# Kernel optimization log

Hardware: AMD Instinct MI355X
Metric: run time of the kernel (lower is better)

The kernel has to match this reference:

```python
import jax, jax.numpy as jnp
import numpy as np

N_NODES = 1_000_000
N_EDGES = 16_000_000
N_FEAT = 128
NUM_GRAPHS = 8192


def setup_inputs() -> dict:
    key = jax.random.key(0)
    k_x, k_e, k_b, k_w, k_pw, k_pb = jax.random.split(key, 6)
    x = jax.random.normal(k_x, (N_NODES, N_FEAT), dtype=jnp.float32)
    edge_index = jax.random.randint(k_e, (2, N_EDGES), 0, N_NODES, dtype=jnp.int64)
    batch = jnp.sort(jax.random.randint(k_b, (N_NODES,), 0, NUM_GRAPHS, dtype=jnp.int64))
    # GCNConv lin weight (F -> 1, no bias), xavier-ish scale
    W = jax.random.normal(k_w, (N_FEAT, 1), dtype=jnp.float32) * (6.0 / (N_FEAT + 1)) ** 0.5
    # post_pool Linear(1, 1, bias=True)
    pp_w = jax.random.normal(k_pw, (1, 1), dtype=jnp.float32)
    pp_b = jax.random.normal(k_pb, (1,), dtype=jnp.float32) * 0.1
    return {"x": x, "W": W, "pp_w": pp_w, "pp_b": pp_b,
            "edge_index": edge_index, "batch": batch}


def reference(x, W, pp_w, pp_b, edge_index, batch):
    N = x.shape[0]
    h = x @ W  # [N, 1] — tiny feature after GCNConv projection
    # add self-loops (PyG GCNConv default)
    loops = jnp.arange(N, dtype=edge_index.dtype)
    src = jnp.concatenate([edge_index[0], loops])  # message sources (col j)
    dst = jnp.concatenate([edge_index[1], loops])  # aggregation targets (row i)
    # symmetric degree normalization: deg over targets incl. self-loops
    deg = jax.ops.segment_sum(jnp.ones(src.shape[0], dtype=h.dtype), dst,
                              num_segments=N)
    dinv = jnp.where(deg > 0, jax.lax.rsqrt(deg), 0.0)
    norm = dinv[src] * dinv[dst]  # [E+N]
    # gather -> normalize -> scatter-add
    agg = jax.ops.segment_sum(norm[:, None] * h[src], dst, num_segments=N)  # [N,1]
    # global_add_pool by graph id
    pooled = jax.ops.segment_sum(agg, batch, num_segments=NUM_GRAPHS)  # [G,1]
    return pooled @ pp_w.T + pp_b  # Linear(1,1)
```

## Files before the change

### kernel.cpp

```cpp
#include <hip/hip_runtime.h>
#include <hip/hip_fp16.h>

#define NUM_GRAPHS 8192
#define BSHIFT 12
#define BSIZE 4096
#define CHUNK 4096
#define NGRP 32

__global__ void node_h_kernel(const float* __restrict__ x,
                              const float* __restrict__ W,
                              float* __restrict__ h, int N) {
    int gwave = (blockIdx.x * blockDim.x + threadIdx.x) >> 6;
    int lane = threadIdx.x & 63;
    int half = lane >> 5;
    int l32  = lane & 31;
    int total_waves = (gridDim.x * blockDim.x) >> 6;
    float4 wv = ((const float4*)W)[l32];
    for (int node = gwave * 2 + half; node < N; node += total_waves * 2) {
        float4 xv = ((const float4*)(x + (size_t)node * 128))[l32];
        float v = xv.x * wv.x + xv.y * wv.y + xv.z * wv.z + xv.w * wv.w;
        #pragma unroll
        for (int d = 16; d >= 1; d >>= 1) v += __shfl_xor(v, d);
        if (l32 == 0) h[node] = v;
    }
}

__global__ void __launch_bounds__(256)
pair_scatter_kernel(const int* __restrict__ src, const int* __restrict__ dst,
                    int E, int nchunks, int NBUK, int capG,
                    unsigned* __restrict__ cursor, unsigned* __restrict__ slab) {
    __shared__ unsigned cnt[256];
    __shared__ unsigned lbase[256];
    __shared__ unsigned sbase[256];
    __shared__ unsigned staged[CHUNK];
    __shared__ unsigned char sbuck[CHUNK];
    __shared__ unsigned s_tot;

    const int4* s4 = (const int4*)src;
    const int4* d4 = (const int4*)dst;
    int E4 = E >> 2;
    int tid = threadIdx.x;
    int g = blockIdx.x & (NGRP - 1);

    for (int chunk = blockIdx.x; chunk < nchunks; chunk += gridDim.x) {
        cnt[tid] = 0; __syncthreads();
        int b4 = chunk * (CHUNK / 4);
        int4 vd[4], vs[4];
        unsigned short r[16];
        #pragma unroll
        for (int k = 0; k < 4; ++k) {
            int idx = b4 + k * 256 + tid;
            if (idx < E4) { vd[k] = d4[idx]; vs[k] = s4[idx]; }
            else          { vd[k] = make_int4(-1, -1, -1, -1); }
        }
        #pragma unroll
        for (int k = 0; k < 4; ++k) {
            if (vd[k].x >= 0) {
                r[4*k+0] = (unsigned short)atomicAdd(&cnt[vd[k].x >> BSHIFT], 1u);
                r[4*k+1] = (unsigned short)atomicAdd(&cnt[vd[k].y >> BSHIFT], 1u);
                r[4*k+2] = (unsigned short)atomicAdd(&cnt[vd[k].z >> BSHIFT], 1u);
                r[4*k+3] = (unsigned short)atomicAdd(&cnt[vd[k].w >> BSHIFT], 1u);
            }
        }
        __syncthreads();
        lbase[tid] = cnt[tid]; __syncthreads();
        #pragma unroll
        for (int off = 1; off < 256; off <<= 1) {
            unsigned a = (tid >= off) ? lbase[tid - off] : 0u;
            __syncthreads();
            lbase[tid] += a;
            __syncthreads();
        }
        if (tid == 255) s_tot = lbase[255];
        if (tid < NBUK && cnt[tid]) sbase[tid] = atomicAdd(&cursor[g * 256 + tid], cnt[tid]);
        unsigned excl = lbase[tid] - cnt[tid];
        __syncthreads();
        lbase[tid] = excl;
        __syncthreads();

        #pragma unroll
        for (int k = 0; k < 4; ++k) {
            if (vd[k].x >= 0) {
                int d0 = vd[k].x, d1 = vd[k].y, d2 = vd[k].z, d3 = vd[k].w;
                unsigned b0 = (unsigned)d0 >> BSHIFT, b1 = (unsigned)d1 >> BSHIFT;
                unsigned b2 = (unsigned)d2 >> BSHIFT, b3 = (unsigned)d3 >> BSHIFT;
                unsigned p0 = lbase[b0] + r[4*k+0];
                unsigned p1 = lbase[b1] + r[4*k+1];
                unsigned p2 = lbase[b2] + r[4*k+2];
                unsigned p3 = lbase[b3] + r[4*k+3];
                staged[p0] = ((unsigned)(d0 & (BSIZE - 1)) << 20) | (unsigned)vs[k].x;
                staged[p1] = ((unsigned)(d1 & (BSIZE - 1)) << 20) | (unsigned)vs[k].y;
                staged[p2] = ((unsigned)(d2 & (BSIZE - 1)) << 20) | (unsigned)vs[k].z;
                staged[p3] = ((unsigned)(d3 & (BSIZE - 1)) << 20) | (unsigned)vs[k].w;
                sbuck[p0] = (unsigned char)b0;
                sbuck[p1] = (unsigned char)b1;
                sbuck[p2] = (unsigned char)b2;
                sbuck[p3] = (unsigned char)b3;
            }
        }
        __syncthreads();

        unsigned tot = s_tot;
        for (unsigned pos = tid; pos < tot; pos += 256) {
            unsigned b = sbuck[pos];
            unsigned gp = sbase[b] + (pos - lbase[b]);
            if (gp < (unsigned)capG)
                slab[((size_t)g * NBUK + b) * capG + gp] = staged[pos];
        }
        __syncthreads();
    }
    if (blockIdx.x == 0 && tid < (E & 3)) {
        int i = (E & ~3) + tid;
        int d = dst[i];
        unsigned b = (unsigned)d >> BSHIFT;
        unsigned p = atomicAdd(&cursor[b], 1u);
        if (p < (unsigned)capG)
            slab[(size_t)b * capG + p] =
                ((unsigned)(d & (BSIZE - 1)) << 20) | (unsigned)src[i];
    }
}

__global__ void __launch_bounds__(1024)
hist_finalize_kernel(const unsigned* __restrict__ slab, int capG,
                     const unsigned* __restrict__ cursor,
                     const float* __restrict__ h, const int* __restrict__ batch,
                     unsigned short* __restrict__ hsh, unsigned* __restrict__ pkw,
                     int N, int NBUK) {
    __shared__ unsigned hist[BSIZE];
    int b = blockIdx.x, tid = threadIdx.x;
    for (int t = tid; t < BSIZE; t += 1024) hist[t] = 0;
    __syncthreads();
    for (int g = 0; g < NGRP; ++g) {
        unsigned n = cursor[g * 256 + b]; if (n > (unsigned)capG) n = capG;
        const unsigned* s = slab + ((size_t)g * NBUK + b) * capG;
        for (unsigned i = tid; i < n; i += 1024) atomicAdd(&hist[s[i] >> 20], 1u);
    }
    __syncthreads();
    int base = b << BSHIFT;
    int lim = N - base; if (lim > BSIZE) lim = BSIZE;
    for (int t = tid; t < lim; t += 1024) {
        float di = rsqrtf((float)(hist[t] + 1u));
        hsh[base + t] = __half_as_ushort(__float2half(di * h[base + t]));
        pkw[base + t] = ((unsigned)batch[base + t] << 16) |
                        __half_as_ushort(__float2half(di));
    }
}

__global__ void __launch_bounds__(1024)
aggregate_kernel(const unsigned* __restrict__ slab, int capG,
                 const unsigned* __restrict__ cursor,
                 const unsigned* __restrict__ pkw,
                 const unsigned short* __restrict__ hsh,
                 float* __restrict__ pooled, int N, int NBUK) {
    __shared__ float pool[NUM_GRAPHS];
    __shared__ unsigned pkw_s[BSIZE];
    int b = blockIdx.x, tid = threadIdx.x;
    int base = b << BSHIFT;
    int lim = N - base; if (lim > BSIZE) lim = BSIZE;

    for (int t = tid; t < NUM_GRAPHS; t += 1024) pool[t] = 0.0f;
    for (int t = tid; t < BSIZE; t += 1024) pkw_s[t] = (t < lim) ? pkw[base + t] : 0u;
    __syncthreads();

    for (int t = tid; t < lim; t += 1024) {
        unsigned w = pkw_s[t];
        float di = __half2float(__ushort_as_half((unsigned short)(w & 0xFFFFu)));
        float c = di * __half2float(__ushort_as_half(hsh[base + t]));
        atomicAdd(&pool[w >> 16], c);
    }

    for (int g = 0; g < NGRP; ++g) {
        unsigned n = cursor[g * 256 + b]; if (n > (unsigned)capG) n = capG;
        const unsigned* s = slab + ((size_t)g * NBUK + b) * capG;
        for (unsigned i = tid; i < n; i += 1024) {
            unsigned e = s[i];
            unsigned w = pkw_s[e >> 20];
            float hv = __half2float(__ushort_as_half(hsh[e & 0xFFFFFu]));
            float di = __half2float(__ushort_as_half((unsigned short)(w & 0xFFFFu)));
            atomicAdd(&pool[w >> 16], hv * di);
        }
    }
    __syncthreads();

    int g_lo = (int)(pkw_s[0] >> 16);
    int g_hi = (lim > 0) ? (int)(pkw_s[lim - 1] >> 16) : g_lo;
    for (int g = g_lo + tid; g <= g_hi; g += 1024) atomicAdd(&pooled[g], pool[g]);
}

__global__ void out_kernel(const float* __restrict__ pooled,
                           const float* __restrict__ pp_w,
                           const float* __restrict__ pp_b,
                           float* __restrict__ out) {
    int g = blockIdx.x * blockDim.x + threadIdx.x;
    if (g < NUM_GRAPHS) out[g] = pooled[g] * pp_w[0] + pp_b[0];
}

__global__ void deg_atomic_kernel(const int* __restrict__ dst, int E,
                                  unsigned* __restrict__ deg) {
    int tid = blockIdx.x * blockDim.x + threadIdx.x;
    int stride = gridDim.x * blockDim.x;
    for (int i = tid; i < E; i += stride) atomicAdd(&deg[dst[i]], 1u);
}

__global__ void node_fb_kernel(const float* __restrict__ x,
                               const float* __restrict__ W,
                               const unsigned* __restrict__ deg,
                               const int* __restrict__ batch,
                               unsigned short* __restrict__ hsh,
                               unsigned* __restrict__ pkw, int N) {
    int gtid = blockIdx.x * blockDim.x + threadIdx.x;
    int wave = gtid >> 6;
    int lane = threadIdx.x & 63;
    int half = lane >> 5;
    int l32  = lane & 31;
    int node = wave * 2 + half;
    if (node >= N) return;
    float4 xv = ((const float4*)(x + (size_t)node * 128))[l32];
    float4 wv = ((const float4*)W)[l32];
    float v = xv.x * wv.x + xv.y * wv.y + xv.z * wv.z + xv.w * wv.w;
// ... 23 lines not shown
                   float* __restrict__ pooled) {
    __shared__ float pool[NUM_GRAPHS];
    for (int g = threadIdx.x; g < NUM_GRAPHS; g += 512) pool[g] = 0.0f;
    __syncthreads();
    int tid = blockIdx.x * 512 + threadIdx.x;
    int stride = gridDim.x * 512;
    for (int i = tid; i < E; i += stride) {
        unsigned w = pkw[dst[i]];
        float c = __half2float(__ushort_as_half(hsh[src[i]])) *
                  __half2float(__ushort_as_half((unsigned short)(w & 0xFFFFu)));
        atomicAdd(&pool[w >> 16], c);
    }
    __syncthreads();
    for (int g = threadIdx.x; g < NUM_GRAPHS; g += 512)
        if (pool[g] != 0.0f) atomicAdd(&pooled[g], pool[g]);
}

extern "C" void kernel_launch(void* const* d_in, const int* in_sizes, int n_in,
                              void* d_out, int out_size, void* d_ws, size_t ws_size,
                              hipStream_t stream) {
    const float* x    = (const float*)d_in[0];
    const float* W    = (const float*)d_in[1];
    const float* pp_w = (const float*)d_in[2];
    const float* pp_b = (const float*)d_in[3];
    const int*   ei   = (const int*)d_in[4];
    const int*   batch= (const int*)d_in[5];
    float* out = (float*)d_out;

    const int E = in_sizes[4] / 2;
    const int N = in_sizes[5];
    const int* src = ei;
    const int* dst = ei + E;
    int NBUK = (N + BSIZE - 1) >> BSHIFT;

    char* ws = (char*)d_ws;
    size_t off = 0;
    auto alloc = [&](size_t bytes) {
        size_t o = off; off = (off + bytes + 255) & ~(size_t)255; return o;
    };
    size_t h_off      = alloc((size_t)N * 4);
    size_t hsh_off    = alloc((size_t)N * 2);
    size_t pkw_off    = alloc((size_t)N * 4);
    size_t pooled_off = alloc((size_t)NUM_GRAPHS * 4);
    size_t cursor_off = alloc((size_t)NGRP * 256 * 4);

    int meanG = E / (NBUK * NGRP) + 1;
    int capG = meanG + meanG / 8 + 512;
    size_t slab_off = alloc((size_t)NGRP * NBUK * (size_t)capG * 4);

    bool slab_ok = (NBUK <= 256) && (N <= (1 << 20)) && (off <= ws_size);

    float*          h      = (float*)(ws + h_off);
    unsigned*       deg    = (unsigned*)(ws + h_off);
    unsigned short* hsh    = (unsigned short*)(ws + hsh_off);
    unsigned*       pkw    = (unsigned*)(ws + pkw_off);
    float*          pooled = (float*)(ws + pooled_off);
    unsigned*       cursor = (unsigned*)(ws + cursor_off);
    unsigned*       slab   = (unsigned*)(ws + slab_off);

    hipMemsetAsync(pooled, 0, (size_t)NUM_GRAPHS * 4, stream);

    if (slab_ok) {
        hipMemsetAsync(cursor, 0, (size_t)NGRP * 256 * 4, stream);
        int E4 = E >> 2;
        int nchunks = (E4 + (CHUNK / 4 - 1)) / (CHUNK / 4);
        int grid = nchunks < 4096 ? nchunks : 4096;
        pair_scatter_kernel<<<grid, 256, 0, stream>>>(src, dst, E, nchunks, NBUK,
                                                      capG, cursor, slab);
        node_h_kernel<<<8192, 256, 0, stream>>>(x, W, h, N);
        hist_finalize_kernel<<<NBUK, 1024, 0, stream>>>(slab, capG, cursor, h,
                                                        batch, hsh, pkw, N, NBUK);
        aggregate_kernel<<<NBUK, 1024, 0, stream>>>(slab, capG, cursor, pkw, hsh,
                                                    pooled, N, NBUK);
    } else {
        hipMemsetAsync(deg, 0, (size_t)N * 4, stream);
        deg_atomic_kernel<<<2048, 256, 0, stream>>>(dst, E, deg);
        int node_blocks = (N + 7) / 8;
        node_fb_kernel<<<node_blocks, 256, 0, stream>>>(x, W, deg, batch, hsh, pkw, N);
        pool_self_fb_kernel<<<(N + 255) / 256, 256, 0, stream>>>(hsh, pkw, pooled, N);
        edge_direct_kernel<<<512, 512, 0, stream>>>(src, dst, E, hsh, pkw, pooled);
    }

    out_kernel<<<(NUM_GRAPHS + 255) / 256, 256, 0, stream>>>(pooled, pp_w, pp_b, out);
}
```

Before: 305.3 us.

## Fuse edge bucketing and node projection into one persistent work-stealing kernel

Merges the edge bucket-scatter kernel and the x@W node projection kernel into a single persistent kernel of 1536 blocks. Each block pulls work from two atomic counters, doing KREP edge chunks and then one node tile in turn, so the latency-bound scatter overlaps with the bandwidth-bound read of x. The two memsets are merged into one over a contiguous zeroed region that also holds the new work counters. The exchange is an extra global atomic per work item and a fixed grid size, and it may change how slab writes are grouped across blocks, since g still comes from blockIdx.

```diff
diff --git a/kernel.cpp b/kernel.cpp
--- a/kernel.cpp
+++ b/kernel.cpp
@@ -6,108 +6,126 @@
 #define BSIZE 4096
 #define CHUNK 4096
 #define NGRP 32
-
-__global__ void node_h_kernel(const float* __restrict__ x,
-                              const float* __restrict__ W,
-                              float* __restrict__ h, int N) {
-    int gwave = (blockIdx.x * blockDim.x + threadIdx.x) >> 6;
-    int lane = threadIdx.x & 63;
-    int half = lane >> 5;
-    int l32  = lane & 31;
-    int total_waves = (gridDim.x * blockDim.x) >> 6;
-    float4 wv = ((const float4*)W)[l32];
-    for (int node = gwave * 2 + half; node < N; node += total_waves * 2) {
-        float4 xv = ((const float4*)(x + (size_t)node * 128))[l32];
-        float v = xv.x * wv.x + xv.y * wv.y + xv.z * wv.z + xv.w * wv.w;
-        #pragma unroll
-        for (int d = 16; d >= 1; d >>= 1) v += __shfl_xor(v, d);
-        if (l32 == 0) h[node] = v;
-    }
-}
+#define HTILE 2048
+#define KREP 8
 
 __global__ void __launch_bounds__(256)
-pair_scatter_kernel(const int* __restrict__ src, const int* __restrict__ dst,
-                    int E, int nchunks, int NBUK, int capG,
-                    unsigned* __restrict__ cursor, unsigned* __restrict__ slab) {
+fused_scatter_h_kernel(const int* __restrict__ src, const int* __restrict__ dst,
+                       int E, int nchunks, int NBUK, int capG,
+                       unsigned* __restrict__ cursor, unsigned* __restrict__ slab,
+                       const float* __restrict__ x, const float* __restrict__ W,
+                       float* __restrict__ h, int N, int ntiles,
+                       unsigned* __restrict__ ccur, unsigned* __restrict__ hcur) {
     __shared__ unsigned cnt[256];
     __shared__ unsigned lbase[256];
     __shared__ unsigned sbase[256];
     __shared__ unsigned staged[CHUNK];
     __shared__ unsigned char sbuck[CHUNK];
     __shared__ unsigned s_tot;
+    __shared__ unsigned s_work;
 
     const int4* s4 = (const int4*)src;
     const int4* d4 = (const int4*)dst;
-    int E4 = E >> 2;
-    int tid = threadIdx.x;
-    int g = blockIdx.x & (NGRP - 1);
-
-    for (int chunk = blockIdx.x; chunk < nchunks; chunk += gridDim.x) {
-        cnt[tid] = 0; __syncthreads();
-        int b4 = chunk * (CHUNK / 4);
-        int4 vd[4], vs[4];
-        unsigned short r[16];
-        #pragma unroll
-        for (int k = 0; k < 4; ++k) {
-            int idx = b4 + k * 256 + tid;
-            if (idx < E4) { vd[k] = d4[idx]; vs[k] = s4[idx]; }
-            else          { vd[k] = make_int4(-1, -1, -1, -1); }
+    const int E4 = E >> 2;
+    const int tid = threadIdx.x;
+    const int g = blockIdx.x & (NGRP - 1);
+
+    const int wv = tid >> 6, hhalf = (tid >> 5) & 1, l32 = tid & 31;
+    const float4 wvec = ((const float4*)W)[l32];
+
+    bool cdone = false, hdone = false;
+    while (!(cdone && hdone)) {
+        for (int rep = 0; rep < KREP && !cdone; ++rep) {
+            if (tid == 0) s_work = atomicAdd(ccur, 1u);
+            __syncthreads();
+            unsigned chunk = s_work;
+            __syncthreads();
+            if (chunk >= (unsigned)nchunks) { cdone = true; continue; }
+
+            cnt[tid] = 0; __syncthreads();
+            int b4 = (int)chunk * (CHUNK / 4);
+            int4 vd[4], vs[4];
+            unsigned short r[16];
+            #pragma unroll
+            for (int k = 0; k < 4; ++k) {
+                int idx = b4 + k * 256 + tid;
+                if (idx < E4) { vd[k] = d4[idx]; vs[k] = s4[idx]; }
+                else          { vd[k] = make_int4(-1, -1, -1, -1); }
+            }
+            #pragma unroll
+            for (int k = 0; k < 4; ++k) {
+                if (vd[k].x >= 0) {
+                    r[4*k+0] = (unsigned short)atomicAdd(&cnt[vd[k].x >> BSHIFT], 1u);
+                    r[4*k+1] = (unsigned short)atomicAdd(&cnt[vd[k].y >> BSHIFT], 1u);
+                    r[4*k+2] = (unsigned short)atomicAdd(&cnt[vd[k].z >> BSHIFT], 1u);
+                    r[4*k+3] = (unsigned short)atomicAdd(&cnt[vd[k].w >> BSHIFT], 1u);
+                }
+            }
+            __syncthreads();
+            lbase[tid] = cnt[tid]; __syncthreads();
+            #pragma unroll
+            for (int off = 1; off < 256; off <<= 1) {
+                unsigned a = (tid >= off) ? lbase[tid - off] : 0u;
+                __syncthreads();
+                lbase[tid] += a;
+                __syncthreads();
+            }
+            if (tid == 255) s_tot = lbase[255];
+            if (tid < NBUK && cnt[tid])
+                sbase[tid] = atomicAdd(&cursor[g * 256 + tid], cnt[tid]);
+            unsigned excl = lbase[tid] - cnt[tid];
+            __syncthreads();
+            lbase[tid] = excl;
+            __syncthreads();
+
+            #pragma unroll
+            for (int k = 0; k < 4; ++k) {
+                if (vd[k].x >= 0) {
+                    int d0 = vd[k].x, d1 = vd[k].y, d2 = vd[k].z, d3 = vd[k].w;
+                    unsigned b0 = (unsigned)d0 >> BSHIFT, b1 = (unsigned)d1 >> BSHIFT;
+                    unsigned b2 = (unsigned)d2 >> BSHIFT, b3 = (unsigned)d3 >> BSHIFT;
+                    unsigned p0 = lbase[b0] + r[4*k+0];
+                    unsigned p1 = lbase[b1] + r[4*k+1];
+                    unsigned p2 = lbase[b2] + r[4*k+2];
+                    unsigned p3 = lbase[b3] + r[4*k+3];
+                    staged[p0] = ((unsigned)(d0 & (BSIZE-1)) << 20) | (unsigned)vs[k].x;
+                    staged[p1] = ((unsigned)(d1 & (BSIZE-1)) << 20) | (unsigned)vs[k].y;
+                    staged[p2] = ((unsigned)(d2 & (BSIZE-1)) << 20) | (unsigned)vs[k].z;
+                    staged[p3] = ((unsigned)(d3 & (BSIZE-1)) << 20) | (unsigned)vs[k].w;
+                    sbuck[p0] = (unsigned char)b0;
+                    sbuck[p1] = (unsigned char)b1;
+                    sbuck[p2] = (unsigned char)b2;
+                    sbuck[p3] = (unsigned char)b3;
+                }
+            }
+            __syncthreads();
+            unsigned tot = s_tot;
+            for (unsigned pos = tid; pos < tot; pos += 256) {
+                unsigned b = sbuck[pos];
+                unsigned gp = sbase[b] + (pos - lbase[b]);
+                if (gp < (unsigned)capG)
+                    slab[((size_t)g * NBUK + b) * capG + gp] = staged[pos];
+            }
+            __syncthreads();
         }
-        #pragma unroll
-        for (int k = 0; k < 4; ++k) {
-            if (vd[k].x >= 0) {
-                r[4*k+0] = (unsigned short)atomicAdd(&cnt[vd[k].x >> BSHIFT], 1u);
-                r[4*k+1] = (unsigned short)atomicAdd(&cnt[vd[k].y >> BSHIFT], 1u);
-                r[4*k+2] = (unsigned short)atomicAdd(&cnt[vd[k].z >> BSHIFT], 1u);
-                r[4*k+3] = (unsigned short)atomicAdd(&cnt[vd[k].w >> BSHIFT], 1u);
+        if (!hdone) {
+            if (tid == 0) s_work = atomicAdd(hcur, 1u);
+            __syncthreads();
+            unsigned t = s_work;
+            __syncthreads();
+            if (t >= (unsigned)ntiles) { hdone = true; continue; }
+            int tbase = (int)t * HTILE;
+            for (int nn = wv * 2 + hhalf; nn < HTILE; nn += 8) {
+                int node = tbase + nn;
+                if (node < N) {
+                    float4 xv = ((const float4*)(x + (size_t)node * 128))[l32];
+                    float v = xv.x*wvec.x + xv.y*wvec.y + xv.z*wvec.z + xv.w*wvec.w;
+                    #pragma unroll
+                    for (int d = 16; d >= 1; d >>= 1) v += __shfl_xor(v, d);
+                    if (l32 == 0) h[node] = v;
+                }
             }
         }
-        __syncthreads();
-        lbase[tid] = cnt[tid]; __syncthreads();
-        #pragma unroll
-        for (int off = 1; off < 256; off <<= 1) {
-            unsigned a = (tid >= off) ? lbase[tid - off] : 0u;
-            __syncthreads();
-            lbase[tid] += a;
-            __syncthreads();
-        }
-        if (tid == 255) s_tot = lbase[255];
-        if (tid < NBUK && cnt[tid]) sbase[tid] = atomicAdd(&cursor[g * 256 + tid], cnt[tid]);
-        unsigned excl = lbase[tid] - cnt[tid];
-        __syncthreads();
-        lbase[tid] = excl;
-        __syncthreads();
-
-        #pragma unroll
-        for (int k = 0; k < 4; ++k) {
-            if (vd[k].x >= 0) {
-                int d0 = vd[k].x, d1 = vd[k].y, d2 = vd[k].z, d3 = vd[k].w;
-                unsigned b0 = (unsigned)d0 >> BSHIFT, b1 = (unsigned)d1 >> BSHIFT;
-                unsigned b2 = (unsigned)d2 >> BSHIFT, b3 = (unsigned)d3 >> BSHIFT;
-                unsigned p0 = lbase[b0] + r[4*k+0];
-                unsigned p1 = lbase[b1] + r[4*k+1];
-                unsigned p2 = lbase[b2] + r[4*k+2];
-                unsigned p3 = lbase[b3] + r[4*k+3];
-                staged[p0] = ((unsigned)(d0 & (BSIZE - 1)) << 20) | (unsigned)vs[k].x;
-                staged[p1] = ((unsigned)(d1 & (BSIZE - 1)) << 20) | (unsigned)vs[k].y;
-                staged[p2] = ((unsigned)(d2 & (BSIZE - 1)) << 20) | (unsigned)vs[k].z;
-                staged[p3] = ((unsigned)(d3 & (BSIZE - 1)) << 20) | (unsigned)vs[k].w;
-                sbuck[p0] = (unsigned char)b0;
-                sbuck[p1] = (unsigned char)b1;
-                sbuck[p2] = (unsigned char)b2;
-                sbuck[p3] = (unsigned char)b3;
-            }
-        }
-        __syncthreads();
-
-        unsigned tot = s_tot;
-        for (unsigned pos = tid; pos < tot; pos += 256) {
-            unsigned b = sbuck[pos];
-            unsigned gp = sbase[b] + (pos - lbase[b]);
-            if (gp < (unsigned)capG)
-                slab[((size_t)g * NBUK + b) * capG + gp] = staged[pos];
-        }
-        __syncthreads();
     }
     if (blockIdx.x == 0 && tid < (E & 3)) {
         int i = (E & ~3) + tid;
@@ -116,7 +134,7 @@
         unsigned p = atomicAdd(&cursor[b], 1u);
         if (p < (unsigned)capG)
             slab[(size_t)b * capG + p] =
-                ((unsigned)(d & (BSIZE - 1)) << 20) | (unsigned)src[i];
+                ((unsigned)(d & (BSIZE-1)) << 20) | (unsigned)src[i];
     }
 }
 
@@ -168,7 +186,6 @@
         float c = di * __half2float(__ushort_as_half(hsh[base + t]));
         atomicAdd(&pool[w >> 16], c);
     }
-
     for (int g = 0; g < NGRP; ++g) {
         unsigned n = cursor[g * 256 + b]; if (n > (unsigned)capG) n = capG;
         const unsigned* s = slab + ((size_t)g * NBUK + b) * capG;
@@ -181,7 +198,6 @@
         }
     }
     __syncthreads();
-
     int g_lo = (int)(pkw_s[0] >> 16);
     int g_hi = (lim > 0) ? (int)(pkw_s[lim - 1] >> 16) : g_lo;
     for (int g = g_lo + tid; g <= g_hi; g += 1024) atomicAdd(&pooled[g], pool[g]);
@@ -280,11 +296,17 @@
     auto alloc = [&](size_t bytes) {
         size_t o = off; off = (off + bytes + 255) & ~(size_t)255; return o;
     };
-    size_t h_off      = alloc((size_t)N * 4);
-    size_t hsh_off    = alloc((size_t)N * 2);
-    size_t pkw_off    = alloc((size_t)N * 4);
-    size_t pooled_off = alloc((size_t)NUM_GRAPHS * 4);
-    size_t cursor_off = alloc((size_t)NGRP * 256 * 4);
+    size_t zero_bytes = (size_t)NUM_GRAPHS * 4 + (size_t)NGRP * 256 * 4 + 256;
+    size_t zero_off   = alloc(zero_bytes);
+    float*    pooled = (float*)(ws + zero_off);
+    unsigned* cursor = (unsigned*)(ws + zero_off + (size_t)NUM_GRAPHS * 4);
+    unsigned* ccur   = (unsigned*)(ws + zero_off + (size_t)NUM_GRAPHS * 4
+                                   + (size_t)NGRP * 256 * 4);
+    unsigned* hcur   = ccur + 1;
+
+    size_t h_off    = alloc((size_t)N * 4);
+    size_t hsh_off  = alloc((size_t)N * 2);
+    size_t pkw_off  = alloc((size_t)N * 4);
 
     int meanG = E / (NBUK * NGRP) + 1;
     int capG = meanG + meanG / 8 + 512;
@@ -292,24 +314,21 @@
 
     bool slab_ok = (NBUK <= 256) && (N <= (1 << 20)) && (off <= ws_size);
 
-    float*          h      = (float*)(ws + h_off);
-    unsigned*       deg    = (unsigned*)(ws + h_off);
-    unsigned short* hsh    = (unsigned short*)(ws + hsh_off);
-    unsigned*       pkw    = (unsigned*)(ws + pkw_off);
-    float*          pooled = (float*)(ws + pooled_off);
-    unsigned*       cursor = (unsigned*)(ws + cursor_off);
-    unsigned*       slab   = (unsigned*)(ws + slab_off);
-
-    hipMemsetAsync(pooled, 0, (size_t)NUM_GRAPHS * 4, stream);
+    float*          h    = (float*)(ws + h_off);
+    unsigned*       deg  = (unsigned*)(ws + h_off);
+    unsigned short* hsh  = (unsigned short*)(ws + hsh_off);
+    unsigned*       pkw  = (unsigned*)(ws + pkw_off);
+    unsigned*       slab = (unsigned*)(ws + slab_off);
+
+    hipMemsetAsync(ws + zero_off, 0, zero_bytes, stream);
 
     if (slab_ok) {
-        hipMemsetAsync(cursor, 0, (size_t)NGRP * 256 * 4, stream);
         int E4 = E >> 2;
         int nchunks = (E4 + (CHUNK / 4 - 1)) / (CHUNK / 4);
-        int grid = nchunks < 4096 ? nchunks : 4096;
-        pair_scatter_kernel<<<grid, 256, 0, stream>>>(src, dst, E, nchunks, NBUK,
-                                                      capG, cursor, slab);
-        node_h_kernel<<<8192, 256, 0, stream>>>(x, W, h, N);
+        int ntiles  = (N + HTILE - 1) / HTILE;
+        fused_scatter_h_kernel<<<1536, 256, 0, stream>>>(
+            src, dst, E, nchunks, NBUK, capG, cursor, slab,
+            x, W, h, N, ntiles, ccur, hcur);
         hist_finalize_kernel<<<NBUK, 1024, 0, stream>>>(slab, capG, cursor, h,
                                                         batch, hsh, pkw, N, NBUK);
         aggregate_kernel<<<NBUK, 1024, 0, stream>>>(slab, capG, cursor, pkw, hsh,
```

After: 437.5 us. 1.43x slower.

## Replace atomic-cursor bucket slabs with deterministic count-scan-scatter partitioning

Applied to the files above, without the earlier changes.

Replaces the single-pass scatter into 32 over-provisioned per-group slabs with a three-stage counting sort. Per-chunk bucket counts are gathered first, then scanned per bucket and globally, and the scatter writes each edge to an exact offset in a compact E-sized slab. The hist and aggregate kernels then read one contiguous range per bucket instead of looping over 32 groups. This drops global cursor atomics, capacity clipping and the slab padding, at the cost of reading dst twice and adding extra small kernel launches. The local prefix scan also moves from a block-wide shared-memory scan to a single-wave shuffle scan.

```diff
diff --git a/kernel.cpp b/kernel.cpp
--- a/kernel.cpp
+++ b/kernel.cpp
@@ -5,7 +5,175 @@
 #define BSHIFT 12
 #define BSIZE 4096
 #define CHUNK 4096
-#define NGRP 32
+#define NTHR 256
+
+__global__ void __launch_bounds__(NTHR)
+count_kernel(const int* __restrict__ dst, int E, int nchunks,
+             unsigned* __restrict__ countsT) {
+    __shared__ unsigned cnt[256];
+    int tid = threadIdx.x;
+    int E4 = E >> 2;
+    const int4* d4 = (const int4*)dst;
+    for (int chunk = blockIdx.x; chunk < nchunks; chunk += gridDim.x) {
+        cnt[tid] = 0; __syncthreads();
+        int b4 = chunk * (CHUNK / 4);
+        #pragma unroll
+        for (int k = 0; k < 4; ++k) {
+            int idx = b4 + k * NTHR + tid;
+            if (idx < E4) {
+                int4 v = d4[idx];
+                atomicAdd(&cnt[v.x >> BSHIFT], 1u);
+                atomicAdd(&cnt[v.y >> BSHIFT], 1u);
+                atomicAdd(&cnt[v.z >> BSHIFT], 1u);
+                atomicAdd(&cnt[v.w >> BSHIFT], 1u);
+            }
+        }
+        if (chunk == nchunks - 1 && tid < (E & 3))
+            atomicAdd(&cnt[dst[E4 * 4 + tid] >> BSHIFT], 1u);
+        __syncthreads();
+        countsT[(size_t)chunk * 256 + tid] = cnt[tid];
+        __syncthreads();
+    }
+}
+
+__global__ void __launch_bounds__(64)
+chunkscan_kernel(const unsigned* __restrict__ countsT, int nchunks,
+                 unsigned* __restrict__ base2T, unsigned* __restrict__ total) {
+    int b = blockIdx.x, lane = threadIdx.x;
+    unsigned run = 0;
+    for (int c0 = 0; c0 < nchunks; c0 += 64) {
+        int c = c0 + lane;
+        unsigned v = (c < nchunks) ? countsT[(size_t)c * 256 + b] : 0u;
+        unsigned s = v;
+        #pragma unroll
+        for (int off = 1; off < 64; off <<= 1) {
+            unsigned o = __shfl_up(s, off);
+            if (lane >= off) s += o;
+        }
+        if (c < nchunks) base2T[(size_t)c * 256 + b] = run + s - v;
+        run += __shfl(s, 63);
+    }
+    if (lane == 0) total[b] = run;
+}
+
+__global__ void gbase_kernel(const unsigned* __restrict__ total,
+                             unsigned* __restrict__ gbase) {
+    __shared__ unsigned s[256];
+    int tid = threadIdx.x;
+    unsigned v = total[tid];
+    s[tid] = v; __syncthreads();
+    #pragma unroll
+    for (int off = 1; off < 256; off <<= 1) {
+        unsigned a = (tid >= off) ? s[tid - off] : 0u;
+        __syncthreads();
+        s[tid] += a;
+        __syncthreads();
+    }
+    gbase[tid] = s[tid] - v;
+    if (tid == 255) gbase[256] = s[255];
+}
+
+__global__ void __launch_bounds__(NTHR)
+scatter_kernel(const int* __restrict__ src, const int* __restrict__ dst,
+               int E, int nchunks,
+               const unsigned* __restrict__ base2T,
+               const unsigned* __restrict__ gbase,
+               unsigned* __restrict__ slab) {
+    __shared__ unsigned cnt[256];
+    __shared__ unsigned lbase[256];
+    __shared__ unsigned sbase[256];
+    __shared__ unsigned staged[CHUNK + 4];
+    __shared__ unsigned char sbuck[CHUNK + 4];
+    __shared__ unsigned s_tot;
+
+    const int4* s4 = (const int4*)src;
+    const int4* d4 = (const int4*)dst;
+    const int E4 = E >> 2;
+    const int tid = threadIdx.x;
+
+    for (int chunk = blockIdx.x; chunk < nchunks; chunk += gridDim.x) {
+        cnt[tid] = 0; __syncthreads();
+        int b4 = chunk * (CHUNK / 4);
+        int4 vd[4], vs[4];
+        unsigned short r[16];
+        #pragma unroll
+        for (int k = 0; k < 4; ++k) {
+            int idx = b4 + k * NTHR + tid;
+            if (idx < E4) { vd[k] = d4[idx]; vs[k] = s4[idx]; }
+            else          { vd[k] = make_int4(-1, -1, -1, -1); }
+        }
+        #pragma unroll
+        for (int k = 0; k < 4; ++k) {
+            if (vd[k].x >= 0) {
+                r[4*k+0] = (unsigned short)atomicAdd(&cnt[vd[k].x >> BSHIFT], 1u);
+                r[4*k+1] = (unsigned short)atomicAdd(&cnt[vd[k].y >> BSHIFT], 1u);
+                r[4*k+2] = (unsigned short)atomicAdd(&cnt[vd[k].z >> BSHIFT], 1u);
+                r[4*k+3] = (unsigned short)atomicAdd(&cnt[vd[k].w >> BSHIFT], 1u);
+            }
+        }
+        int tr = -1, tsrc = 0, tdlo = 0, tb = 0;
+        if (chunk == nchunks - 1 && tid < (E & 3)) {
+            int i = E4 * 4 + tid;
+            int d = dst[i];
+            tb = d >> BSHIFT;
+            tr = (int)atomicAdd(&cnt[tb], 1u);
+            tdlo = d & (BSIZE - 1);
+            tsrc = src[i];
+        }
+        __syncthreads();
+        sbase[tid] = gbase[tid] + base2T[(size_t)chunk * 256 + tid];
+        if (tid < 64) {
+            unsigned run = 0;
+            for (int c0 = 0; c0 < 256; c0 += 64) {
+                unsigned v = cnt[c0 + tid];
+                unsigned s = v;
+                #pragma unroll
+                for (int off = 1; off < 64; off <<= 1) {
+                    unsigned o = __shfl_up(s, off);
+                    if (tid >= off) s += o;
+                }
+                lbase[c0 + tid] = run + s - v;
+                run += __shfl(s, 63);
+            }
+            if (tid == 0) s_tot = run;
+        }
+        __syncthreads();
+
+        #pragma unroll
+        for (int k = 0; k < 4; ++k) {
+            if (vd[k].x >= 0) {
+                int d0 = vd[k].x, d1 = vd[k].y, d2 = vd[k].z, d3 = vd[k].w;
+                unsigned b0 = (unsigned)d0 >> BSHIFT, b1 = (unsigned)d1 >> BSHIFT;
+                unsigned b2 = (unsigned)d2 >> BSHIFT, b3 = (unsigned)d3 >> BSHIFT;
+                unsigned p0 = lbase[b0] + r[4*k+0];
+                unsigned p1 = lbase[b1] + r[4*k+1];
+                unsigned p2 = lbase[b2] + r[4*k+2];
+                unsigned p3 = lbase[b3] + r[4*k+3];
+                staged[p0] = ((unsigned)(d0 & (BSIZE-1)) << 20) | (unsigned)vs[k].x;
+                staged[p1] = ((unsigned)(d1 & (BSIZE-1)) << 20) | (unsigned)vs[k].y;
+                staged[p2] = ((unsigned)(d2 & (BSIZE-1)) << 20) | (unsigned)vs[k].z;
+                staged[p3] = ((unsigned)(d3 & (BSIZE-1)) << 20) | (unsigned)vs[k].w;
+                sbuck[p0] = (unsigned char)b0;
+                sbuck[p1] = (unsigned char)b1;
+                sbuck[p2] = (unsigned char)b2;
+                sbuck[p3] = (unsigned char)b3;
+            }
+        }
+        if (tr >= 0) {
+            unsigned p = lbase[tb] + (unsigned)tr;
+            staged[p] = ((unsigned)tdlo << 20) | (unsigned)tsrc;
+            sbuck[p] = (unsigned char)tb;
+        }
+        __syncthreads();
+
+        unsigned tot = s_tot;
+        for (unsigned pos = tid; pos < tot; pos += NTHR) {
+            unsigned b = sbuck[pos];
+            slab[sbase[b] + (pos - lbase[b])] = staged[pos];
+        }
+        __syncthreads();
+    }
+}
 
 __global__ void node_h_kernel(const float* __restrict__ x,
                               const float* __restrict__ W,
@@ -25,116 +193,19 @@
     }
 }
 
-__global__ void __launch_bounds__(256)
-pair_scatter_kernel(const int* __restrict__ src, const int* __restrict__ dst,
-                    int E, int nchunks, int NBUK, int capG,
-                    unsigned* __restrict__ cursor, unsigned* __restrict__ slab) {
-    __shared__ unsigned cnt[256];
-    __shared__ unsigned lbase[256];
-    __shared__ unsigned sbase[256];
-    __shared__ unsigned staged[CHUNK];
-    __shared__ unsigned char sbuck[CHUNK];
-    __shared__ unsigned s_tot;
-
-    const int4* s4 = (const int4*)src;
-    const int4* d4 = (const int4*)dst;
-    int E4 = E >> 2;
-    int tid = threadIdx.x;
-    int g = blockIdx.x & (NGRP - 1);
-
-    for (int chunk = blockIdx.x; chunk < nchunks; chunk += gridDim.x) {
-        cnt[tid] = 0; __syncthreads();
-        int b4 = chunk * (CHUNK / 4);
-        int4 vd[4], vs[4];
-        unsigned short r[16];
-        #pragma unroll
-        for (int k = 0; k < 4; ++k) {
-            int idx = b4 + k * 256 + tid;
-            if (idx < E4) { vd[k] = d4[idx]; vs[k] = s4[idx]; }
-            else          { vd[k] = make_int4(-1, -1, -1, -1); }
-        }
-        #pragma unroll
-        for (int k = 0; k < 4; ++k) {
-            if (vd[k].x >= 0) {
-                r[4*k+0] = (unsigned short)atomicAdd(&cnt[vd[k].x >> BSHIFT], 1u);
-                r[4*k+1] = (unsigned short)atomicAdd(&cnt[vd[k].y >> BSHIFT], 1u);
-                r[4*k+2] = (unsigned short)atomicAdd(&cnt[vd[k].z >> BSHIFT], 1u);
-                r[4*k+3] = (unsigned short)atomicAdd(&cnt[vd[k].w >> BSHIFT], 1u);
-            }
-        }
-        __syncthreads();
-        lbase[tid] = cnt[tid]; __syncthreads();
-        #pragma unroll
-        for (int off = 1; off < 256; off <<= 1) {
-            unsigned a = (tid >= off) ? lbase[tid - off] : 0u;
-            __syncthreads();
-            lbase[tid] += a;
-            __syncthreads();
-        }
-        if (tid == 255) s_tot = lbase[255];
-        if (tid < NBUK && cnt[tid]) sbase[tid] = atomicAdd(&cursor[g * 256 + tid], cnt[tid]);
-        unsigned excl = lbase[tid] - cnt[tid];
-        __syncthreads();
-        lbase[tid] = excl;
-        __syncthreads();
-
-        #pragma unroll
-        for (int k = 0; k < 4; ++k) {
-            if (vd[k].x >= 0) {
-                int d0 = vd[k].x, d1 = vd[k].y, d2 = vd[k].z, d3 = vd[k].w;
-                unsigned b0 = (unsigned)d0 >> BSHIFT, b1 = (unsigned)d1 >> BSHIFT;
-                unsigned b2 = (unsigned)d2 >> BSHIFT, b3 = (unsigned)d3 >> BSHIFT;
-                unsigned p0 = lbase[b0] + r[4*k+0];
-                unsigned p1 = lbase[b1] + r[4*k+1];
-                unsigned p2 = lbase[b2] + r[4*k+2];
-                unsigned p3 = lbase[b3] + r[4*k+3];
-                staged[p0] = ((unsigned)(d0 & (BSIZE - 1)) << 20) | (unsigned)vs[k].x;
-                staged[p1] = ((unsigned)(d1 & (BSIZE - 1)) << 20) | (unsigned)vs[k].y;
-                staged[p2] = ((unsigned)(d2 & (BSIZE - 1)) << 20) | (unsigned)vs[k].z;
-                staged[p3] = ((unsigned)(d3 & (BSIZE - 1)) << 20) | (unsigned)vs[k].w;
-                sbuck[p0] = (unsigned char)b0;
-                sbuck[p1] = (unsigned char)b1;
-                sbuck[p2] = (unsigned char)b2;
-                sbuck[p3] = (unsigned char)b3;
-            }
-        }
-        __syncthreads();
-
-        unsigned tot = s_tot;
-        for (unsigned pos = tid; pos < tot; pos += 256) {
-            unsigned b = sbuck[pos];
-            unsigned gp = sbase[b] + (pos - lbase[b]);
-            if (gp < (unsigned)capG)
-                slab[((size_t)g * NBUK + b) * capG + gp] = staged[pos];
-        }
-        __syncthreads();
-    }
-    if (blockIdx.x == 0 && tid < (E & 3)) {
-        int i = (E & ~3) + tid;
-        int d = dst[i];
-        unsigned b = (unsigned)d >> BSHIFT;
-        unsigned p = atomicAdd(&cursor[b], 1u);
-        if (p < (unsigned)capG)
-            slab[(size_t)b * capG + p] =
-                ((unsigned)(d & (BSIZE - 1)) << 20) | (unsigned)src[i];
-    }
-}
-
 __global__ void __launch_bounds__(1024)
-hist_finalize_kernel(const unsigned* __restrict__ slab, int capG,
-                     const unsigned* __restrict__ cursor,
+hist_finalize_kernel(const unsigned* __restrict__ slab,
+                     const unsigned* __restrict__ gbase,
                      const float* __restrict__ h, const int* __restrict__ batch,
                      unsigned short* __restrict__ hsh, unsigned* __restrict__ pkw,
-                     int N, int NBUK) {
+                     int N) {
     __shared__ unsigned hist[BSIZE];
     int b = blockIdx.x, tid = threadIdx.x;
     for (int t = tid; t < BSIZE; t += 1024) hist[t] = 0;
     __syncthreads();
-    for (int g = 0; g < NGRP; ++g) {
-        unsigned n = cursor[g * 256 + b]; if (n > (unsigned)capG) n = capG;
-        const unsigned* s = slab + ((size_t)g * NBUK + b) * capG;
-        for (unsigned i = tid; i < n; i += 1024) atomicAdd(&hist[s[i] >> 20], 1u);
-    }
+    unsigned s0 = gbase[b], s1 = gbase[b + 1];
+    for (unsigned i = s0 + tid; i < s1; i += 1024)
+        atomicAdd(&hist[slab[i] >> 20], 1u);
     __syncthreads();
     int base = b << BSHIFT;
     int lim = N - base; if (lim > BSIZE) lim = BSIZE;
@@ -147,11 +218,11 @@
 }
 
 __global__ void __launch_bounds__(1024)
-aggregate_kernel(const unsigned* __restrict__ slab, int capG,
-                 const unsigned* __restrict__ cursor,
+aggregate_kernel(const unsigned* __restrict__ slab,
+                 const unsigned* __restrict__ gbase,
                  const unsigned* __restrict__ pkw,
                  const unsigned short* __restrict__ hsh,
-                 float* __restrict__ pooled, int N, int NBUK) {
+                 float* __restrict__ pooled, int N) {
     __shared__ float pool[NUM_GRAPHS];
     __shared__ unsigned pkw_s[BSIZE];
     int b = blockIdx.x, tid = threadIdx.x;
@@ -168,20 +239,15 @@
         float c = di * __half2float(__ushort_as_half(hsh[base + t]));
         atomicAdd(&pool[w >> 16], c);
     }
-
-    for (int g = 0; g < NGRP; ++g) {
-        unsigned n = cursor[g * 256 + b]; if (n > (unsigned)capG) n = capG;
-        const unsigned* s = slab + ((size_t)g * NBUK + b) * capG;
-        for (unsigned i = tid; i < n; i += 1024) {
-            unsigned e = s[i];
-            unsigned w = pkw_s[e >> 20];
-            float hv = __half2float(__ushort_as_half(hsh[e & 0xFFFFFu]));
-            float di = __half2float(__ushort_as_half((unsigned short)(w & 0xFFFFu)));
-            atomicAdd(&pool[w >> 16], hv * di);
-        }
-    }
-    __syncthreads();
-
+    unsigned s0 = gbase[b], s1 = gbase[b + 1];
+    for (unsigned i = s0 + tid; i < s1; i += 1024) {
+        unsigned e = slab[i];
+        unsigned w = pkw_s[e >> 20];
+        float hv = __half2float(__ushort_as_half(hsh[e & 0xFFFFFu]));
+        float di = __half2float(__ushort_as_half((unsigned short)(w & 0xFFFFu)));
+        atomicAdd(&pool[w >> 16], hv * di);
+    }
+    __syncthreads();
     int g_lo = (int)(pkw_s[0] >> 16);
     int g_hi = (lim > 0) ? (int)(pkw_s[lim - 1] >> 16) : g_lo;
     for (int g = g_lo + tid; g <= g_hi; g += 1024) atomicAdd(&pooled[g], pool[g]);
@@ -274,46 +340,50 @@
     const int* src = ei;
     const int* dst = ei + E;
     int NBUK = (N + BSIZE - 1) >> BSHIFT;
+    int nchunks = (E + CHUNK - 1) / CHUNK;
 
     char* ws = (char*)d_ws;
     size_t off = 0;
     auto alloc = [&](size_t bytes) {
         size_t o = off; off = (off + bytes + 255) & ~(size_t)255; return o;
     };
+    size_t pooled_off = alloc((size_t)NUM_GRAPHS * 4);
     size_t h_off      = alloc((size_t)N * 4);
     size_t hsh_off    = alloc((size_t)N * 2);
     size_t pkw_off    = alloc((size_t)N * 4);
-    size_t pooled_off = alloc((size_t)NUM_GRAPHS * 4);
-    size_t cursor_off = alloc((size_t)NGRP * 256 * 4);
-
-    int meanG = E / (NBUK * NGRP) + 1;
-    int capG = meanG + meanG / 8 + 512;
-    size_t slab_off = alloc((size_t)NGRP * NBUK * (size_t)capG * 4);
-
-    bool slab_ok = (NBUK <= 256) && (N <= (1 << 20)) && (off <= ws_size);
-
+    size_t counts_off = alloc((size_t)nchunks * 256 * 4);
+    size_t base2_off  = alloc((size_t)nchunks * 256 * 4);
+    size_t total_off  = alloc(256 * 4);
+    size_t gbase_off  = alloc(257 * 4);
+    size_t slab_off   = alloc((size_t)E * 4);
+
+    bool fast_ok = (NBUK <= 256) && (N <= (1 << 20)) && (off <= ws_size);
+
+    float*          pooled = (float*)(ws + pooled_off);
     float*          h      = (float*)(ws + h_off);
     unsigned*       deg    = (unsigned*)(ws + h_off);
     unsigned short* hsh    = (unsigned short*)(ws + hsh_off);
     unsigned*       pkw    = (unsigned*)(ws + pkw_off);
-    float*          pooled = (float*)(ws + pooled_off);
-    unsigned*       cursor = (unsigned*)(ws + cursor_off);
+    unsigned*       countsT= (unsigned*)(ws + counts_off);
+    unsigned*       base2T = (unsigned*)(ws + base2_off);
+    unsigned*       total  = (unsigned*)(ws + total_off);
+    unsigned*       gbase  = (unsigned*)(ws + gbase_off);
     unsigned*       slab   = (unsigned*)(ws + slab_off);
 
     hipMemsetAsync(pooled, 0, (size_t)NUM_GRAPHS * 4, stream);
 
-    if (slab_ok) {
-        hipMemsetAsync(cursor, 0, (size_t)NGRP * 256 * 4, stream);
-        int E4 = E >> 2;
-        int nchunks = (E4 + (CHUNK / 4 - 1)) / (CHUNK / 4);
-        int grid = nchunks < 4096 ? nchunks : 4096;
-        pair_scatter_kernel<<<grid, 256, 0, stream>>>(src, dst, E, nchunks, NBUK,
-                                                      capG, cursor, slab);
+    if (fast_ok) {
+        int grid_c = nchunks < 2048 ? nchunks : 2048;
+        count_kernel<<<grid_c, NTHR, 0, stream>>>(dst, E, nchunks, countsT);
+        chunkscan_kernel<<<256, 64, 0, stream>>>(countsT, nchunks, base2T, total);
+        gbase_kernel<<<1, 256, 0, stream>>>(total, gbase);
+        scatter_kernel<<<grid_c, NTHR, 0, stream>>>(src, dst, E, nchunks,
+                                                    base2T, gbase, slab);
         node_h_kernel<<<8192, 256, 0, stream>>>(x, W, h, N);
-        hist_finalize_kernel<<<NBUK, 1024, 0, stream>>>(slab, capG, cursor, h,
-                                                        batch, hsh, pkw, N, NBUK);
-        aggregate_kernel<<<NBUK, 1024, 0, stream>>>(slab, capG, cursor, pkw, hsh,
-                                                    pooled, N, NBUK);
+        hist_finalize_kernel<<<NBUK, 1024, 0, stream>>>(slab, gbase, h, batch,
+                                                        hsh, pkw, N);
+        aggregate_kernel<<<NBUK, 1024, 0, stream>>>(slab, gbase, pkw, hsh,
+                                                    pooled, N);
     } else {
         hipMemsetAsync(deg, 0, (size_t)N * 4, stream);
         deg_atomic_kernel<<<2048, 256, 0, stream>>>(dst, E, deg);
```

Result: slower. 351.8 us (+15.2%).

## Split histogram and aggregation across more blocks, fuse projection with normalization

Applied to the files above, without the earlier changes.

The degree histogram now runs in two blocks per bucket, each covering half the slab groups and writing partial degrees to two arrays. The node projection is fused with the rsqrt normalization and packing, so the separate h buffer and its round trip are gone. Aggregation runs four blocks per bucket with 8-way batched slab loads and gathers, and accumulates into a small replicated, padded shared-memory window of graph ids in place of a full 8192-entry pool. The aim is more parallelism over the ~245 buckets and less shared-atomic contention, at the cost of extra global atomics and a non-windowed fallback path.

```diff
diff --git a/kernel.cpp b/kernel.cpp
--- a/kernel.cpp
+++ b/kernel.cpp
@@ -6,24 +6,9 @@
 #define BSIZE 4096
 #define CHUNK 4096
 #define NGRP 32
-
-__global__ void node_h_kernel(const float* __restrict__ x,
-                              const float* __restrict__ W,
-                              float* __restrict__ h, int N) {
-    int gwave = (blockIdx.x * blockDim.x + threadIdx.x) >> 6;
-    int lane = threadIdx.x & 63;
-    int half = lane >> 5;
-    int l32  = lane & 31;
-    int total_waves = (gridDim.x * blockDim.x) >> 6;
-    float4 wv = ((const float4*)W)[l32];
-    for (int node = gwave * 2 + half; node < N; node += total_waves * 2) {
-        float4 xv = ((const float4*)(x + (size_t)node * 128))[l32];
-        float v = xv.x * wv.x + xv.y * wv.y + xv.z * wv.z + xv.w * wv.w;
-        #pragma unroll
-        for (int d = 16; d >= 1; d >>= 1) v += __shfl_xor(v, d);
-        if (l32 == 0) h[node] = v;
-    }
-}
+#define REPL 8
+#define WINDOW 256
+#define WPAD 257
 
 __global__ void __launch_bounds__(256)
 pair_scatter_kernel(const int* __restrict__ src, const int* __restrict__ dst,
@@ -72,7 +57,8 @@
             __syncthreads();
         }
         if (tid == 255) s_tot = lbase[255];
-        if (tid < NBUK && cnt[tid]) sbase[tid] = atomicAdd(&cursor[g * 256 + tid], cnt[tid]);
+        if (tid < NBUK && cnt[tid])
+            sbase[tid] = atomicAdd(&cursor[g * 256 + tid], cnt[tid]);
         unsigned excl = lbase[tid] - cnt[tid];
         __syncthreads();
         lbase[tid] = excl;
@@ -88,10 +74,10 @@
                 unsigned p1 = lbase[b1] + r[4*k+1];
                 unsigned p2 = lbase[b2] + r[4*k+2];
                 unsigned p3 = lbase[b3] + r[4*k+3];
-                staged[p0] = ((unsigned)(d0 & (BSIZE - 1)) << 20) | (unsigned)vs[k].x;
-                staged[p1] = ((unsigned)(d1 & (BSIZE - 1)) << 20) | (unsigned)vs[k].y;
-                staged[p2] = ((unsigned)(d2 & (BSIZE - 1)) << 20) | (unsigned)vs[k].z;
-                staged[p3] = ((unsigned)(d3 & (BSIZE - 1)) << 20) | (unsigned)vs[k].w;
+                staged[p0] = ((unsigned)(d0 & (BSIZE-1)) << 20) | (unsigned)vs[k].x;
+                staged[p1] = ((unsigned)(d1 & (BSIZE-1)) << 20) | (unsigned)vs[k].y;
+                staged[p2] = ((unsigned)(d2 & (BSIZE-1)) << 20) | (unsigned)vs[k].z;
+                staged[p3] = ((unsigned)(d3 & (BSIZE-1)) << 20) | (unsigned)vs[k].w;
                 sbuck[p0] = (unsigned char)b0;
                 sbuck[p1] = (unsigned char)b1;
                 sbuck[p2] = (unsigned char)b2;
@@ -99,7 +85,6 @@
             }
         }
         __syncthreads();
-
         unsigned tot = s_tot;
         for (unsigned pos = tid; pos < tot; pos += 256) {
             unsigned b = sbuck[pos];
@@ -116,75 +101,145 @@
         unsigned p = atomicAdd(&cursor[b], 1u);
         if (p < (unsigned)capG)
             slab[(size_t)b * capG + p] =
-                ((unsigned)(d & (BSIZE - 1)) << 20) | (unsigned)src[i];
-    }
-}
-
-__global__ void __launch_bounds__(1024)
-hist_finalize_kernel(const unsigned* __restrict__ slab, int capG,
-                     const unsigned* __restrict__ cursor,
-                     const float* __restrict__ h, const int* __restrict__ batch,
-                     unsigned short* __restrict__ hsh, unsigned* __restrict__ pkw,
-                     int N, int NBUK) {
+                ((unsigned)(d & (BSIZE-1)) << 20) | (unsigned)src[i];
+    }
+}
+
+__global__ void __launch_bounds__(512)
+hist_kernel(const unsigned* __restrict__ slab, int capG,
+            const unsigned* __restrict__ cursor,
+            unsigned* __restrict__ deg0, unsigned* __restrict__ deg1,
+            int N, int NBUK) {
     __shared__ unsigned hist[BSIZE];
-    int b = blockIdx.x, tid = threadIdx.x;
-    for (int t = tid; t < BSIZE; t += 1024) hist[t] = 0;
-    __syncthreads();
-    for (int g = 0; g < NGRP; ++g) {
-        unsigned n = cursor[g * 256 + b]; if (n > (unsigned)capG) n = capG;
-        const unsigned* s = slab + ((size_t)g * NBUK + b) * capG;
-        for (unsigned i = tid; i < n; i += 1024) atomicAdd(&hist[s[i] >> 20], 1u);
+    int bp = blockIdx.x, tid = threadIdx.x;
+    int b = bp >> 1, half = bp & 1;
+    for (int t = tid; t < BSIZE; t += 512) hist[t] = 0;
+    __syncthreads();
+
+    int g0 = half * 16;
+    for (int gg = g0; gg < g0 + 16; gg += 8) {
+        unsigned n[8], maxn = 0;
+        const unsigned* sp[8];
+        #pragma unroll
+        for (int k = 0; k < 8; ++k) {
+            unsigned nn = cursor[(gg + k) * 256 + b];
+            if (nn > (unsigned)capG) nn = capG;
+            n[k] = nn; if (nn > maxn) maxn = nn;
+            sp[k] = slab + ((size_t)(gg + k) * NBUK + b) * capG;
+        }
+        for (unsigned i = tid; i < maxn; i += 512) {
+            unsigned e[8];
+            #pragma unroll
+            for (int k = 0; k < 8; ++k) e[k] = (i < n[k]) ? sp[k][i] : 0xFFFFFFFFu;
+            #pragma unroll
+            for (int k = 0; k < 8; ++k)
+                if (e[k] != 0xFFFFFFFFu) atomicAdd(&hist[e[k] >> 20], 1u);
+        }
     }
     __syncthreads();
     int base = b << BSHIFT;
     int lim = N - base; if (lim > BSIZE) lim = BSIZE;
-    for (int t = tid; t < lim; t += 1024) {
-        float di = rsqrtf((float)(hist[t] + 1u));
-        hsh[base + t] = __half_as_ushort(__float2half(di * h[base + t]));
-        pkw[base + t] = ((unsigned)batch[base + t] << 16) |
+    unsigned* degP = half ? deg1 : deg0;
+    for (int t = tid; t < lim; t += 512) degP[base + t] = hist[t];
+}
+
+__global__ void node_kernel(const float* __restrict__ x,
+                            const float* __restrict__ W,
+                            const unsigned* __restrict__ deg0,
+                            const unsigned* __restrict__ deg1,
+                            const int* __restrict__ batch,
+                            unsigned short* __restrict__ hsh,
+                            unsigned* __restrict__ pkw, int N) {
+    int gwave = (blockIdx.x * blockDim.x + threadIdx.x) >> 6;
+    int lane = threadIdx.x & 63;
+    int half = lane >> 5;
+    int l32  = lane & 31;
+    int total_waves = (gridDim.x * blockDim.x) >> 6;
+    float4 wv = ((const float4*)W)[l32];
+    for (int node = gwave * 2 + half; node < N; node += total_waves * 2) {
+        float4 xv = ((const float4*)(x + (size_t)node * 128))[l32];
+        float v = xv.x * wv.x + xv.y * wv.y + xv.z * wv.z + xv.w * wv.w;
+        #pragma unroll
+        for (int d = 16; d >= 1; d >>= 1) v += __shfl_xor(v, d);
+        if (l32 == 0) {
+            float di = rsqrtf((float)(deg0[node] + deg1[node] + 1u));
+            hsh[node] = __half_as_ushort(__float2half(di * v));
+            pkw[node] = ((unsigned)batch[node] << 16) |
                         __half_as_ushort(__float2half(di));
-    }
-}
-
-__global__ void __launch_bounds__(1024)
+        }
+    }
+}
+
+__global__ void __launch_bounds__(512)
 aggregate_kernel(const unsigned* __restrict__ slab, int capG,
                  const unsigned* __restrict__ cursor,
                  const unsigned* __restrict__ pkw,
                  const unsigned short* __restrict__ hsh,
                  float* __restrict__ pooled, int N, int NBUK) {
-    __shared__ float pool[NUM_GRAPHS];
     __shared__ unsigned pkw_s[BSIZE];
-    int b = blockIdx.x, tid = threadIdx.x;
+    __shared__ float win[REPL * WPAD];
+    int bp = blockIdx.x, tid = threadIdx.x;
+    int b = bp >> 2, q = bp & 3;
     int base = b << BSHIFT;
     int lim = N - base; if (lim > BSIZE) lim = BSIZE;
 
-    for (int t = tid; t < NUM_GRAPHS; t += 1024) pool[t] = 0.0f;
-    for (int t = tid; t < BSIZE; t += 1024) pkw_s[t] = (t < lim) ? pkw[base + t] : 0u;
-    __syncthreads();
-
-    for (int t = tid; t < lim; t += 1024) {
+    for (int t = tid; t < BSIZE; t += 512) pkw_s[t] = (t < lim) ? pkw[base + t] : 0u;
+    for (int t = tid; t < REPL * WPAD; t += 512) win[t] = 0.0f;
+    __syncthreads();
+    int g_lo = (int)(pkw_s[0] >> 16);
+    int g_hi = (lim > 0) ? (int)(pkw_s[lim - 1] >> 16) : g_lo;
+    int width = g_hi - g_lo + 1;
+    bool windowed = (width <= WINDOW);
+    int r = tid & (REPL - 1);
+
+    int n0 = q * (BSIZE / 4);
+    int n1 = (q + 1) * (BSIZE / 4); if (n1 > lim) n1 = lim;
+    for (int t = n0 + tid; t < n1; t += 512) {
         unsigned w = pkw_s[t];
         float di = __half2float(__ushort_as_half((unsigned short)(w & 0xFFFFu)));
         float c = di * __half2float(__ushort_as_half(hsh[base + t]));
-        atomicAdd(&pool[w >> 16], c);
-    }
-
-    for (int g = 0; g < NGRP; ++g) {
-        unsigned n = cursor[g * 256 + b]; if (n > (unsigned)capG) n = capG;
-        const unsigned* s = slab + ((size_t)g * NBUK + b) * capG;
-        for (unsigned i = tid; i < n; i += 1024) {
-            unsigned e = s[i];
-            unsigned w = pkw_s[e >> 20];
-            float hv = __half2float(__ushort_as_half(hsh[e & 0xFFFFFu]));
-            float di = __half2float(__ushort_as_half((unsigned short)(w & 0xFFFFu)));
-            atomicAdd(&pool[w >> 16], hv * di);
-        }
-    }
-    __syncthreads();
-
-    int g_lo = (int)(pkw_s[0] >> 16);
-    int g_hi = (lim > 0) ? (int)(pkw_s[lim - 1] >> 16) : g_lo;
-    for (int g = g_lo + tid; g <= g_hi; g += 1024) atomicAdd(&pooled[g], pool[g]);
+        if (windowed) atomicAdd(&win[r * WPAD + ((w >> 16) - g_lo)], c);
+        else          atomicAdd(&pooled[w >> 16], c);
+    }
+
+    int g0 = q * 8;
+    unsigned n[8], maxn = 0;
+    const unsigned* sp[8];
+    #pragma unroll
+    for (int k = 0; k < 8; ++k) {
+        unsigned nn = cursor[(g0 + k) * 256 + b];
+        if (nn > (unsigned)capG) nn = capG;
+        n[k] = nn; if (nn > maxn) maxn = nn;
+        sp[k] = slab + ((size_t)(g0 + k) * NBUK + b) * capG;
+    }
+    for (unsigned i = tid; i < maxn; i += 512) {
+        unsigned e[8]; bool v[8];
+        #pragma unroll
+        for (int k = 0; k < 8; ++k) { v[k] = (i < n[k]); e[k] = v[k] ? sp[k][i] : 0u; }
+        unsigned w[8];
+        #pragma unroll
+        for (int k = 0; k < 8; ++k) w[k] = pkw_s[e[k] >> 20];
+        unsigned short hb[8];
+        #pragma unroll
+        for (int k = 0; k < 8; ++k) hb[k] = hsh[e[k] & 0xFFFFFu];
+        #pragma unroll
+        for (int k = 0; k < 8; ++k) {
+            float hv = __half2float(__ushort_as_half(hb[k]));
+            float di = __half2float(__ushort_as_half((unsigned short)(w[k] & 0xFFFFu)));
+            float c = v[k] ? hv * di : 0.0f;
+            if (windowed) atomicAdd(&win[r * WPAD + ((w[k] >> 16) - g_lo)], c);
+            else if (v[k]) atomicAdd(&pooled[w[k] >> 16], c);
+        }
+    }
+    __syncthreads();
+    if (windowed) {
+        for (int g = tid; g < width; g += 512) {
+            float s = 0.0f;
+            #pragma unroll
+            for (int rr = 0; rr < REPL; ++rr) s += win[rr * WPAD + g];
+            atomicAdd(&pooled[g_lo + g], s);
+        }
+    }
 }
 
 __global__ void out_kernel(const float* __restrict__ pooled,
@@ -274,51 +329,51 @@
     const int* src = ei;
     const int* dst = ei + E;
     int NBUK = (N + BSIZE - 1) >> BSHIFT;
+    int nchunks = (E + CHUNK - 1) / CHUNK;
 
     char* ws = (char*)d_ws;
     size_t off = 0;
     auto alloc = [&](size_t bytes) {
         size_t o = off; off = (off + bytes + 255) & ~(size_t)255; return o;
     };
-    size_t h_off      = alloc((size_t)N * 4);
-    size_t hsh_off    = alloc((size_t)N * 2);
-    size_t pkw_off    = alloc((size_t)N * 4);
-    size_t pooled_off = alloc((size_t)NUM_GRAPHS * 4);
-    size_t cursor_off = alloc((size_t)NGRP * 256 * 4);
+    size_t zero_bytes = (size_t)NUM_GRAPHS * 4 + (size_t)NGRP * 256 * 4;
+    size_t zero_off   = alloc(zero_bytes);
+    float*    pooled = (float*)(ws + zero_off);
+    unsigned* cursor = (unsigned*)(ws + zero_off + (size_t)NUM_GRAPHS * 4);
+
+    size_t deg0_off = alloc((size_t)N * 4);
+    size_t deg1_off = alloc((size_t)N * 4);
+    size_t hsh_off  = alloc((size_t)N * 2);
+    size_t pkw_off  = alloc((size_t)N * 4);
 
     int meanG = E / (NBUK * NGRP) + 1;
-    int capG = meanG + meanG / 8 + 512;
+    int capG = (meanG + meanG / 8 + 512 + 3) & ~3;
     size_t slab_off = alloc((size_t)NGRP * NBUK * (size_t)capG * 4);
 
-    bool slab_ok = (NBUK <= 256) && (N <= (1 << 20)) && (off <= ws_size);
-
-    float*          h      = (float*)(ws + h_off);
-    unsigned*       deg    = (unsigned*)(ws + h_off);
-    unsigned short* hsh    = (unsigned short*)(ws + hsh_off);
-    unsigned*       pkw    = (unsigned*)(ws + pkw_off);
-    float*          pooled = (float*)(ws + pooled_off);
-    unsigned*       cursor = (unsigned*)(ws + cursor_off);
-    unsigned*       slab   = (unsigned*)(ws + slab_off);
-
-    hipMemsetAsync(pooled, 0, (size_t)NUM_GRAPHS * 4, stream);
-
-    if (slab_ok) {
-        hipMemsetAsync(cursor, 0, (size_t)NGRP * 256 * 4, stream);
-        int E4 = E >> 2;
-        int nchunks = (E4 + (CHUNK / 4 - 1)) / (CHUNK / 4);
+    bool fast_ok = (NBUK <= 256) && (N <= (1 << 20)) && (off <= ws_size);
+
+    unsigned*       deg0 = (unsigned*)(ws + deg0_off);
+    unsigned*       deg1 = (unsigned*)(ws + deg1_off);
+    unsigned short* hsh  = (unsigned short*)(ws + hsh_off);
+    unsigned*       pkw  = (unsigned*)(ws + pkw_off);
+    unsigned*       slab = (unsigned*)(ws + slab_off);
+
+    hipMemsetAsync(ws + zero_off, 0, zero_bytes, stream);
+
+    if (fast_ok) {
         int grid = nchunks < 4096 ? nchunks : 4096;
         pair_scatter_kernel<<<grid, 256, 0, stream>>>(src, dst, E, nchunks, NBUK,
                                                       capG, cursor, slab);
-        node_h_kernel<<<8192, 256, 0, stream>>>(x, W, h, N);
-        hist_finalize_kernel<<<NBUK, 1024, 0, stream>>>(slab, capG, cursor, h,
-                                                        batch, hsh, pkw, N, NBUK);
-        aggregate_kernel<<<NBUK, 1024, 0, stream>>>(slab, capG, cursor, pkw, hsh,
-                                                    pooled, N, NBUK);
+        hist_kernel<<<2 * NBUK, 512, 0, stream>>>(slab, capG, cursor,
+                                                  deg0, deg1, N, NBUK);
+        node_kernel<<<8192, 256, 0, stream>>>(x, W, deg0, deg1, batch, hsh, pkw, N);
+        aggregate_kernel<<<4 * NBUK, 512, 0, stream>>>(slab, capG, cursor, pkw,
+                                                       hsh, pooled, N, NBUK);
     } else {
-        hipMemsetAsync(deg, 0, (size_t)N * 4, stream);
-        deg_atomic_kernel<<<2048, 256, 0, stream>>>(dst, E, deg);
+        hipMemsetAsync(deg0, 0, (size_t)N * 4, stream);
+        deg_atomic_kernel<<<2048, 256, 0, stream>>>(dst, E, deg0);
         int node_blocks = (N + 7) / 8;
-        node_fb_kernel<<<node_blocks, 256, 0, stream>>>(x, W, deg, batch, hsh, pkw, N);
+        node_fb_kernel<<<node_blocks, 256, 0, stream>>>(x, W, deg0, batch, hsh, pkw, N);
         pool_self_fb_kernel<<<(N + 255) / 256, 256, 0, stream>>>(hsh, pkw, pooled, N);
         edge_direct_kernel<<<512, 512, 0, stream>>>(src, dst, E, hsh, pkw, pooled);
     }
```

Result: faster. 292.5 us (-4.2%).
